# Performance work log

Measured on AMD Instinct MI355X. Metric: run time of the kernel, lower is better.

The kernel has to match this reference:

```python
import jax, jax.numpy as jnp
import numpy as np

TEMPERATURE = 0.5
EPS = 1e-8  # torch CosineSimilarity eps


def setup_inputs() -> dict:
    key = jax.random.key(0)
    k1, k2 = jax.random.split(key)
    N, D = 4096, 256
    z1 = jax.random.normal(k1, (N, D), dtype=jnp.float32)
    z2 = jax.random.normal(k2, (N, D), dtype=jnp.float32)
    return {"z1": z1, "z2": z2}


def reference(z1, z2):
    N = z1.shape[0]
    z = jnp.concatenate([z1, z2], axis=0)  # [2N, D]
    # cosine similarity = normalized dot products (GEMM instead of O(N^2 D) broadcast)
    norm = jnp.linalg.norm(z, axis=-1, keepdims=True)
    zn = z / jnp.maximum(norm, EPS)
    sim = (zn @ zn.T) / TEMPERATURE  # [2N, 2N]
    # mask self-similarity on the diagonal
    idx = jnp.arange(2 * N)
    sim = jnp.where(idx[:, None] == idx[None, :], -jnp.inf, sim)
    # target[i] = (i - N) mod 2N  (arange(2N).roll(N))
    target = jnp.roll(idx, N)
    logp = jax.nn.log_softmax(sim, axis=-1)
    loss = -jnp.mean(logp[idx, target])
    return loss
```

## Files before the change

### kernel.cpp

```cpp
#include <hip/hip_runtime.h>

typedef __bf16 bf16x8 __attribute__((ext_vector_type(8)));
typedef float f32x4 __attribute__((ext_vector_type(4)));

#define TWO_LOG2E 2.88539008177792681f

#define GLOADLDS16(g, l) __builtin_amdgcn_global_load_lds(                     \
    (const __attribute__((address_space(1))) void*)(g),                        \
    (__attribute__((address_space(3))) void*)(l), 16, 0, 0)

__device__ __forceinline__ unsigned short f2bf(float f) {
    unsigned int u = __float_as_uint(f);
    u = (u + 0x7FFFu + ((u >> 16) & 1u)) >> 16;
    return (unsigned short)u;
}

__global__ void normalize_kernel(const float* __restrict__ z1,
                                 const float* __restrict__ z2,
                                 unsigned short* __restrict__ zn) {
    const int wave = threadIdx.x >> 6, lane = threadIdx.x & 63;
    const int row = (blockIdx.x << 2) + wave;
    const float* src = (row < 4096) ? (z1 + row * 256) : (z2 + (row - 4096) * 256);
    float4 v = ((const float4*)src)[lane];
    float ss = v.x * v.x + v.y * v.y + v.z * v.z + v.w * v.w;
#pragma unroll
    for (int m = 32; m > 0; m >>= 1) ss += __shfl_xor(ss, m, 64);
    float scale = 1.0f / fmaxf(sqrtf(ss), 1e-8f);
    uint2 w;
    w.x = (unsigned)f2bf(v.x * scale) | ((unsigned)f2bf(v.y * scale) << 16);
    w.y = (unsigned)f2bf(v.z * scale) | ((unsigned)f2bf(v.w * scale) << 16);
    *(uint2*)(zn + row * 256 + (lane << 2)) = w;
}

__global__ void __launch_bounds__(256) simexp_kernel(
    const unsigned short* __restrict__ zn,
    float* __restrict__ S)
{
    __shared__ __align__(16) unsigned short As[128 * 64];
    __shared__ __align__(16) unsigned short Bs[128 * 64];

    const int tid  = threadIdx.x;
    const int lane = tid & 63;
    const int wave = tid >> 6;
    const int wr = wave >> 1;
    const int wc = wave & 1;
    const int q   = lane >> 4;
    const int n16 = lane & 15;

    int t = blockIdx.x, bi = 0;
    while (t >= 64 - bi) { t -= 64 - bi; ++bi; }
    const int bj = bi + t;
    const int rowBase = bi << 7;
    const int colBase = bj << 7;

    const int lrow = lane >> 3;
    const int k8s  = (lane & 7) ^ lrow;

    f32x4 acc[4][4];
#pragma unroll
    for (int i = 0; i < 4; ++i)
#pragma unroll
        for (int j = 0; j < 4; ++j) acc[i][j] = (f32x4){0.f, 0.f, 0.f, 0.f};

    for (int kc = 0; kc < 4; ++kc) {
        __syncthreads();
#pragma unroll
        for (int p = 0; p < 4; ++p) {
            const int seg = (wave << 2) + p;
            const int r = (seg << 3) + lrow;
            const unsigned short* ga = zn + ((rowBase + r) << 8) + (kc << 6) + (k8s << 3);
            const unsigned short* gb = zn + ((colBase + r) << 8) + (kc << 6) + (k8s << 3);
            GLOADLDS16(ga, As + (seg << 9) + (lane << 3));
            GLOADLDS16(gb, Bs + (seg << 9) + (lane << 3));
        }
        __syncthreads();
#pragma unroll
        for (int ks = 0; ks < 2; ++ks) {
            bf16x8 af[4], bfr[4];
#pragma unroll
            for (int rt = 0; rt < 4; ++rt) {
                const int ar = (wr << 6) + (rt << 4) + n16;
                const int kk = ((ks << 2) + q) ^ (n16 & 7);
                af[rt] = *(const bf16x8*)(As + (ar << 6) + (kk << 3));
            }
#pragma unroll
            for (int ct = 0; ct < 4; ++ct) {
                const int br = (wc << 6) + (ct << 4) + n16;
                const int kk = ((ks << 2) + q) ^ (n16 & 7);
                bfr[ct] = *(const bf16x8*)(Bs + (br << 6) + (kk << 3));
            }
#pragma unroll
            for (int rt = 0; rt < 4; ++rt)
#pragma unroll
                for (int ct = 0; ct < 4; ++ct)
                    acc[rt][ct] = __builtin_amdgcn_mfma_f32_16x16x32_bf16(
                        af[rt], bfr[ct], acc[rt][ct], 0, 0, 0);
        }
    }

    float rs[4][4];
    float cs[4];
#pragma unroll
    for (int i = 0; i < 4; ++i) {
        cs[i] = 0.f;
#pragma unroll
        for (int j = 0; j < 4; ++j) rs[i][j] = 0.f;
    }
#pragma unroll
    for (int rt = 0; rt < 4; ++rt)
#pragma unroll
        for (int ct = 0; ct < 4; ++ct)
#pragma unroll
            for (int r = 0; r < 4; ++r) {
                float e = __builtin_amdgcn_exp2f(acc[rt][ct][r] * TWO_LOG2E);
                rs[rt][r] += e;
                cs[ct] += e;
            }

#pragma unroll
    for (int rt = 0; rt < 4; ++rt)
#pragma unroll
        for (int r = 0; r < 4; ++r) {
            float s = rs[rt][r];
            s += __shfl_xor(s, 1, 64);
            s += __shfl_xor(s, 2, 64);
            s += __shfl_xor(s, 4, 64);
            s += __shfl_xor(s, 8, 64);
            if (n16 == 0) {
                int grow = rowBase + (wr << 6) + (rt << 4) + (q << 2) + r;
                atomicAdd(&S[grow], s);
            }
        }
    if (bi != bj) {
#pragma unroll
        for (int ct = 0; ct < 4; ++ct) {
            float s = cs[ct];
            s += __shfl_xor(s, 16, 64);
            s += __shfl_xor(s, 32, 64);
            if (q == 0) {
                int gcol = colBase + (wc << 6) + (ct << 4) + n16;
                atomicAdd(&S[gcol], s);
            }
        }
    }
}

__global__ void finish_kernel(const unsigned short* __restrict__ zn,
                              const float* __restrict__ S,
                              float* __restrict__ out)
{
    __shared__ float vals[16];
    const int tid = threadIdx.x, lane = tid & 63, wave = tid >> 6;
    const int rib = (wave << 2) + (lane >> 4);
    const int row = (blockIdx.x << 4) + rib;
    const int tar = (row + 4096) & 8191;
    const int l16 = lane & 15;

    float drr = 0.f, drt = 0.f;
#pragma unroll
    for (int i = 0; i < 4; ++i) {
        int k = (i << 6) + (l16 << 2);
        uint2 ur = *(const uint2*)(zn + (row << 8) + k);
        uint2 ut = *(const uint2*)(zn + (tar << 8) + k);
        float a0 = __uint_as_float(ur.x << 16);
        float a1 = __uint_as_float(ur.x & 0xFFFF0000u);
        float a2 = __uint_as_float(ur.y << 16);
        float a3 = __uint_as_float(ur.y & 0xFFFF0000u);
        float b0 = __uint_as_float(ut.x << 16);
        float b1 = __uint_as_float(ut.x & 0xFFFF0000u);
        float b2 = __uint_as_float(ut.y << 16);
        float b3 = __uint_as_float(ut.y & 0xFFFF0000u);
        drr += a0 * a0 + a1 * a1 + a2 * a2 + a3 * a3;
        drt += a0 * b0 + a1 * b1 + a2 * b2 + a3 * b3;
    }
#pragma unroll
    for (int m = 1; m <= 8; m <<= 1) {
        drr += __shfl_xor(drr, m, 64);
        drt += __shfl_xor(drt, m, 64);
    }
    if (l16 == 0) {
        float Sv = S[row] - __builtin_amdgcn_exp2f(drr * TWO_LOG2E);
        vals[rib] = 0.693147180559945f * __builtin_amdgcn_logf(Sv) - 2.0f * drt;
    }
    __syncthreads();
    if (tid == 0) {
        float s = 0.f;
#pragma unroll
        for (int i = 0; i < 16; ++i) s += vals[i];
        atomicAdd(out, s * (1.0f / 8192.0f));
    }
}

extern "C" void kernel_launch(void* const* d_in, const int* in_sizes, int n_in,
                              void* d_out, int out_size, void* d_ws, size_t ws_size,
                              hipStream_t stream)
{
    const float* z1 = (const float*)d_in[0];
    const float* z2 = (const float*)d_in[1];
    unsigned short* zn = (unsigned short*)d_ws;
    float* S = (float*)((char*)d_ws + 8192 * 256 * sizeof(unsigned short));
    float* out = (float*)d_out;

    hipMemsetAsync(S, 0, 8192 * sizeof(float), stream);
    hipMemsetAsync(out, 0, sizeof(float), stream);

    normalize_kernel<<<2048, 256, 0, stream>>>(z1, z2, zn);
    simexp_kernel<<<2080, 256, 0, stream>>>(zn, S);
    finish_kernel<<<512, 256, 0, stream>>>(zn, S, out);
}
```

Measured before the change: 126.0 us.

## Fuse normalize, similarity-exp, and finish into one persistent cooperative kernel

Replaces three kernel launches and two memsets with one cooperative persistent kernel that uses grid syncs between phases, with a non-cooperative fallback. The GEMM phase now gives each block a contiguous range of 128x64 upper-triangle tiles. A-rows stay in registers per strip, B tiles are double-buffered in LDS with prefetch, and row sums are flushed only on strip change, which cuts atomics. The aim is to remove launch and memset overhead and to improve load balance and latency hiding. In exchange it adds grid-sync costs, higher register pressure from holding A in registers, and host-side device queries on every call.

```diff
diff --git a/kernel.cpp b/kernel.cpp
--- a/kernel.cpp
+++ b/kernel.cpp
@@ -1,4 +1,7 @@
 #include <hip/hip_runtime.h>
+#include <hip/hip_cooperative_groups.h>
+
+namespace cg = cooperative_groups;
 
 typedef __bf16 bf16x8 __attribute__((ext_vector_type(8)));
 typedef float f32x4 __attribute__((ext_vector_type(4)));
@@ -9,186 +12,246 @@
     (const __attribute__((address_space(1))) void*)(g),                        \
     (__attribute__((address_space(3))) void*)(l), 16, 0, 0)
 
-__device__ __forceinline__ unsigned short f2bf(float f) {
-    unsigned int u = __float_as_uint(f);
-    u = (u + 0x7FFFu + ((u >> 16) & 1u)) >> 16;
-    return (unsigned short)u;
-}
-
-__global__ void normalize_kernel(const float* __restrict__ z1,
-                                 const float* __restrict__ z2,
-                                 unsigned short* __restrict__ zn) {
-    const int wave = threadIdx.x >> 6, lane = threadIdx.x & 63;
-    const int row = (blockIdx.x << 2) + wave;
-    const float* src = (row < 4096) ? (z1 + row * 256) : (z2 + (row - 4096) * 256);
-    float4 v = ((const float4*)src)[lane];
-    float ss = v.x * v.x + v.y * v.y + v.z * v.z + v.w * v.w;
-#pragma unroll
-    for (int m = 32; m > 0; m >>= 1) ss += __shfl_xor(ss, m, 64);
-    float scale = 1.0f / fmaxf(sqrtf(ss), 1e-8f);
-    uint2 w;
-    w.x = (unsigned)f2bf(v.x * scale) | ((unsigned)f2bf(v.y * scale) << 16);
-    w.y = (unsigned)f2bf(v.z * scale) | ((unsigned)f2bf(v.w * scale) << 16);
-    *(uint2*)(zn + row * 256 + (lane << 2)) = w;
-}
-
-__global__ void __launch_bounds__(256) simexp_kernel(
-    const unsigned short* __restrict__ zn,
-    float* __restrict__ S)
-{
-    __shared__ __align__(16) unsigned short As[128 * 64];
-    __shared__ __align__(16) unsigned short Bs[128 * 64];
-
-    const int tid  = threadIdx.x;
-    const int lane = tid & 63;
-    const int wave = tid >> 6;
-    const int wr = wave >> 1;
-    const int wc = wave & 1;
-    const int q   = lane >> 4;
-    const int n16 = lane & 15;
-
-    int t = blockIdx.x, bi = 0;
-    while (t >= 64 - bi) { t -= 64 - bi; ++bi; }
-    const int bj = bi + t;
-    const int rowBase = bi << 7;
-    const int colBase = bj << 7;
-
-    const int lrow = lane >> 3;
-    const int k8s  = (lane & 7) ^ lrow;
-
-    f32x4 acc[4][4];
+__device__ __forceinline__ unsigned f2bf(float f) {
+    unsigned u = __float_as_uint(f);
+    return (u + 0x7FFFu + ((u >> 16) & 1u)) >> 16;
+}
+
+__device__ __forceinline__ void phase1(const float* __restrict__ z1,
+                                       const float* __restrict__ z2,
+                                       unsigned short* __restrict__ zn,
+                                       float* __restrict__ S,
+                                       float* __restrict__ out) {
+    const int tid = threadIdx.x, lane = tid & 63, wave = tid >> 6;
+    for (int grp = blockIdx.x; grp < 512; grp += gridDim.x) {
+        if (tid < 16) S[(grp << 4) + tid] = 0.f;
+        if (grp == 0 && tid == 0) out[0] = 0.f;
+#pragma unroll
+        for (int r = 0; r < 4; ++r) {
+            int row = (grp << 4) + (wave << 2) + r;
+            const float* src = (row < 4096) ? (z1 + row * 256) : (z2 + (row - 4096) * 256);
+            float4 v = ((const float4*)src)[lane];
+            float ss = v.x * v.x + v.y * v.y + v.z * v.z + v.w * v.w;
+#pragma unroll
+            for (int m = 32; m > 0; m >>= 1) ss += __shfl_xor(ss, m, 64);
+            float sc = 1.0f / fmaxf(sqrtf(ss), 1e-8f);
+            uint2 w;
+            w.x = f2bf(v.x * sc) | (f2bf(v.y * sc) << 16);
+            w.y = f2bf(v.z * sc) | (f2bf(v.w * sc) << 16);
+            *(uint2*)(zn + row * 256 + (lane << 2)) = w;
+        }
+    }
+}
+
+__device__ __forceinline__ void phase2(const unsigned short* __restrict__ zn,
+                                       float* __restrict__ S,
+                                       unsigned short* __restrict__ Bs) {
+    const int tid = threadIdx.x, lane = tid & 63, wave = tid >> 6;
+    const int q = lane >> 4, n16 = lane & 15;
+    const int wr = wave >> 1, wc = wave & 1;
+    const int G = gridDim.x, b = blockIdx.x;
+
+    const int gs = (b * 4160) / G;
+    const int ge = ((b + 1) * 4160) / G;
+
+    int si = 0;
+    while ((si + 1) * (128 - si) <= gs) ++si;
+    int ti = gs - si * (129 - si);
+
+    auto stage = [&](int colBase, int h, int buf) {
+        unsigned short* base = Bs + (buf << 13);
+#pragma unroll
+        for (int p = 0; p < 4; ++p) {
+            int s16 = (p << 8) + tid;
+            int c   = s16 >> 4;
+            int k8  = (s16 & 15) ^ (c & 15);
+            GLOADLDS16(zn + ((colBase + c) << 8) + (h << 7) + (k8 << 3),
+                       base + (s16 << 3));
+        }
+    };
+
+    bf16x8 a[4][8];
+    auto loadA = [&](int rb) {
+#pragma unroll
+        for (int rt = 0; rt < 4; ++rt)
+#pragma unroll
+            for (int ks = 0; ks < 8; ++ks)
+                a[rt][ks] = *(const bf16x8*)(zn + ((rb + (wr << 6) + (rt << 4) + n16) << 8)
+                                                + (ks << 5) + (q << 3));
+    };
+
+    float rs[4][4];
 #pragma unroll
     for (int i = 0; i < 4; ++i)
 #pragma unroll
-        for (int j = 0; j < 4; ++j) acc[i][j] = (f32x4){0.f, 0.f, 0.f, 0.f};
-
-    for (int kc = 0; kc < 4; ++kc) {
-        __syncthreads();
-#pragma unroll
-        for (int p = 0; p < 4; ++p) {
-            const int seg = (wave << 2) + p;
-            const int r = (seg << 3) + lrow;
-            const unsigned short* ga = zn + ((rowBase + r) << 8) + (kc << 6) + (k8s << 3);
-            const unsigned short* gb = zn + ((colBase + r) << 8) + (kc << 6) + (k8s << 3);
-            GLOADLDS16(ga, As + (seg << 9) + (lane << 3));
-            GLOADLDS16(gb, Bs + (seg << 9) + (lane << 3));
-        }
-        __syncthreads();
-#pragma unroll
-        for (int ks = 0; ks < 2; ++ks) {
-            bf16x8 af[4], bfr[4];
-#pragma unroll
-            for (int rt = 0; rt < 4; ++rt) {
-                const int ar = (wr << 6) + (rt << 4) + n16;
-                const int kk = ((ks << 2) + q) ^ (n16 & 7);
-                af[rt] = *(const bf16x8*)(As + (ar << 6) + (kk << 3));
+        for (int j = 0; j < 4; ++j) rs[i][j] = 0.f;
+
+    auto flushRows = [&](int strip) {
+        int base = (strip << 7) + (wr << 6) + (q << 2);
+#pragma unroll
+        for (int rt = 0; rt < 4; ++rt)
+#pragma unroll
+            for (int r = 0; r < 4; ++r) {
+                float s = rs[rt][r];
+                s += __shfl_xor(s, 1, 64);
+                s += __shfl_xor(s, 2, 64);
+                s += __shfl_xor(s, 4, 64);
+                s += __shfl_xor(s, 8, 64);
+                if (n16 == 0) atomicAdd(&S[base + (rt << 4) + r], s);
+                rs[rt][r] = 0.f;
             }
-#pragma unroll
-            for (int ct = 0; ct < 4; ++ct) {
-                const int br = (wc << 6) + (ct << 4) + n16;
-                const int kk = ((ks << 2) + q) ^ (n16 & 7);
-                bfr[ct] = *(const bf16x8*)(Bs + (br << 6) + (kk << 3));
+    };
+
+    loadA(si << 7);
+    int curStrip = si;
+    stage((si << 7) + (ti << 6), 0, 0);
+    int pi = si, pt = ti, ph = 0;
+    int buf = 0;
+
+    for (int g = gs; g < ge; ++g) {
+        if (si != curStrip) { flushRows(curStrip); loadA(si << 7); curStrip = si; }
+        const int rowBase = si << 7;
+        const int colBase = rowBase + (ti << 6);
+
+        f32x4 acc[4][2];
+#pragma unroll
+        for (int rt = 0; rt < 4; ++rt)
+#pragma unroll
+            for (int ct = 0; ct < 2; ++ct) acc[rt][ct] = (f32x4){0.f, 0.f, 0.f, 0.f};
+
+#pragma unroll
+        for (int h = 0; h < 2; ++h) {
+            __syncthreads();
+            ph ^= 1;
+            if (ph == 0) { ++pt; if (pt >= 128 - (pi << 1)) { ++pi; pt = 0; } }
+            if (pi < 64) stage((pi << 7) + (pt << 6), ph, buf ^ 1);
+
+            const unsigned short* bb = Bs + (buf << 13);
+#pragma unroll
+            for (int ksl = 0; ksl < 4; ++ksl) {
+                bf16x8 bf[2];
+#pragma unroll
+                for (int ct = 0; ct < 2; ++ct) {
+                    int c  = (wc << 5) + (ct << 4) + n16;
+                    int k8 = ((ksl << 2) | q) ^ n16;
+                    bf[ct] = *(const bf16x8*)(bb + (((c << 4) | k8) << 3));
+                }
+#pragma unroll
+                for (int rt = 0; rt < 4; ++rt)
+#pragma unroll
+                    for (int ct = 0; ct < 2; ++ct)
+                        acc[rt][ct] = __builtin_amdgcn_mfma_f32_16x16x32_bf16(
+                            a[rt][(h << 2) + ksl], bf[ct], acc[rt][ct], 0, 0, 0);
             }
-#pragma unroll
-            for (int rt = 0; rt < 4; ++rt)
-#pragma unroll
-                for (int ct = 0; ct < 4; ++ct)
-                    acc[rt][ct] = __builtin_amdgcn_mfma_f32_16x16x32_bf16(
-                        af[rt], bfr[ct], acc[rt][ct], 0, 0, 0);
-        }
-    }
-
-    float rs[4][4];
-    float cs[4];
-#pragma unroll
-    for (int i = 0; i < 4; ++i) {
-        cs[i] = 0.f;
-#pragma unroll
-        for (int j = 0; j < 4; ++j) rs[i][j] = 0.f;
-    }
-#pragma unroll
-    for (int rt = 0; rt < 4; ++rt)
-#pragma unroll
-        for (int ct = 0; ct < 4; ++ct)
-#pragma unroll
-            for (int r = 0; r < 4; ++r) {
-                float e = __builtin_amdgcn_exp2f(acc[rt][ct][r] * TWO_LOG2E);
-                rs[rt][r] += e;
-                cs[ct] += e;
-            }
-
-#pragma unroll
-    for (int rt = 0; rt < 4; ++rt)
-#pragma unroll
-        for (int r = 0; r < 4; ++r) {
-            float s = rs[rt][r];
-            s += __shfl_xor(s, 1, 64);
-            s += __shfl_xor(s, 2, 64);
-            s += __shfl_xor(s, 4, 64);
-            s += __shfl_xor(s, 8, 64);
-            if (n16 == 0) {
-                int grow = rowBase + (wr << 6) + (rt << 4) + (q << 2) + r;
-                atomicAdd(&S[grow], s);
-            }
-        }
-    if (bi != bj) {
-#pragma unroll
-        for (int ct = 0; ct < 4; ++ct) {
+            buf ^= 1;
+        }
+
+        float cs[2] = {0.f, 0.f};
+        const bool strad = (ti < 2);
+        const int ibase = rowBase + (wr << 6) + (q << 2);
+        const int jb    = colBase + (wc << 5) + n16;
+#pragma unroll
+        for (int rt = 0; rt < 4; ++rt)
+#pragma unroll
+            for (int ct = 0; ct < 2; ++ct)
+#pragma unroll
+                for (int r = 0; r < 4; ++r) {
+                    float e = __builtin_amdgcn_exp2f(acc[rt][ct][r] * TWO_LOG2E);
+                    if (strad) {
+                        int ii = ibase + (rt << 4) + r;
+                        int jj = jb + (ct << 4);
+                        rs[rt][r] += (jj >= ii) ? e : 0.f;
+                        cs[ct]    += (jj >  ii) ? e : 0.f;
+                    } else {
+                        rs[rt][r] += e;
+                        cs[ct]    += e;
+                    }
+                }
+#pragma unroll
+        for (int ct = 0; ct < 2; ++ct) {
             float s = cs[ct];
             s += __shfl_xor(s, 16, 64);
             s += __shfl_xor(s, 32, 64);
-            if (q == 0) {
-                int gcol = colBase + (wc << 6) + (ct << 4) + n16;
-                atomicAdd(&S[gcol], s);
-            }
-        }
-    }
-}
-
-__global__ void finish_kernel(const unsigned short* __restrict__ zn,
-                              const float* __restrict__ S,
-                              float* __restrict__ out)
+            if (q == 0) atomicAdd(&S[colBase + (wc << 5) + (ct << 4) + n16], s);
+        }
+        ++ti; if (ti >= 128 - (si << 1)) { ++si; ti = 0; }
+    }
+    flushRows(curStrip);
+}
+
+__device__ __forceinline__ void phase3(const unsigned short* __restrict__ zn,
+                                       const float* __restrict__ S,
+                                       float* __restrict__ out,
+                                       float* __restrict__ vals) {
+    const int tid = threadIdx.x, lane = tid & 63, wave = tid >> 6;
+    const int q = lane >> 4, n16 = lane & 15;
+    const int rib = (wave << 2) + q;
+    for (int grp = blockIdx.x; grp < 512; grp += gridDim.x) {
+        int row = (grp << 4) + rib;
+        int tar = (row + 4096) & 8191;
+        float drr = 0.f, drt = 0.f;
+#pragma unroll
+        for (int i = 0; i < 4; ++i) {
+            int k = (i << 6) + (n16 << 2);
+            uint2 ur = *(const uint2*)(zn + (row << 8) + k);
+            uint2 ut = *(const uint2*)(zn + (tar << 8) + k);
+            float a0 = __uint_as_float(ur.x << 16),  a1 = __uint_as_float(ur.x & 0xFFFF0000u);
+            float a2 = __uint_as_float(ur.y << 16),  a3 = __uint_as_float(ur.y & 0xFFFF0000u);
+            float b0 = __uint_as_float(ut.x << 16),  b1 = __uint_as_float(ut.x & 0xFFFF0000u);
+            float b2 = __uint_as_float(ut.y << 16),  b3 = __uint_as_float(ut.y & 0xFFFF0000u);
+            drr += a0 * a0 + a1 * a1 + a2 * a2 + a3 * a3;
+            drt += a0 * b0 + a1 * b1 + a2 * b2 + a3 * b3;
+        }
+#pragma unroll
+        for (int m = 1; m <= 8; m <<= 1) {
+            drr += __shfl_xor(drr, m, 64);
+            drt += __shfl_xor(drt, m, 64);
+        }
+        __syncthreads();
+        if (n16 == 0) {
+            float Sv = S[row] - __builtin_amdgcn_exp2f(drr * TWO_LOG2E);
+            vals[rib] = 0.693147180559945f * __builtin_amdgcn_logf(Sv) - 2.0f * drt;
+        }
+        __syncthreads();
+        if (tid == 0) {
+            float s = 0.f;
+#pragma unroll
+            for (int i = 0; i < 16; ++i) s += vals[i];
+            atomicAdd(out, s * (1.0f / 8192.0f));
+        }
+    }
+}
+
+__global__ void __launch_bounds__(256, 2) ntxent_fused(
+    const float* __restrict__ z1, const float* __restrict__ z2,
+    unsigned short* __restrict__ zn, float* __restrict__ S, float* __restrict__ out)
+{
+    __shared__ __align__(16) unsigned short Bs[2][8192];
+    phase1(z1, z2, zn, S, out);
+    cg::this_grid().sync();
+    phase2(zn, S, &Bs[0][0]);
+    cg::this_grid().sync();
+    phase3(zn, S, out, (float*)&Bs[0][0]);
+}
+
+__global__ void __launch_bounds__(256, 2) norm_k(
+    const float* __restrict__ z1, const float* __restrict__ z2,
+    unsigned short* __restrict__ zn, float* __restrict__ S, float* __restrict__ out)
+{ phase1(z1, z2, zn, S, out); }
+
+__global__ void __launch_bounds__(256, 2) simexp_k(
+    const unsigned short* __restrict__ zn, float* __restrict__ S)
+{
+    __shared__ __align__(16) unsigned short Bs[2][8192];
+    phase2(zn, S, &Bs[0][0]);
+}
+
+__global__ void __launch_bounds__(256, 2) finish_k(
+    const unsigned short* __restrict__ zn, const float* __restrict__ S,
+    float* __restrict__ out)
 {
     __shared__ float vals[16];
-    const int tid = threadIdx.x, lane = tid & 63, wave = tid >> 6;
-    const int rib = (wave << 2) + (lane >> 4);
-    const int row = (blockIdx.x << 4) + rib;
-    const int tar = (row + 4096) & 8191;
-    const int l16 = lane & 15;
-
-    float drr = 0.f, drt = 0.f;
-#pragma unroll
-    for (int i = 0; i < 4; ++i) {
-        int k = (i << 6) + (l16 << 2);
-        uint2 ur = *(const uint2*)(zn + (row << 8) + k);
-        uint2 ut = *(const uint2*)(zn + (tar << 8) + k);
-        float a0 = __uint_as_float(ur.x << 16);
-        float a1 = __uint_as_float(ur.x & 0xFFFF0000u);
-        float a2 = __uint_as_float(ur.y << 16);
-        float a3 = __uint_as_float(ur.y & 0xFFFF0000u);
-        float b0 = __uint_as_float(ut.x << 16);
-        float b1 = __uint_as_float(ut.x & 0xFFFF0000u);
-        float b2 = __uint_as_float(ut.y << 16);
-        float b3 = __uint_as_float(ut.y & 0xFFFF0000u);
-        drr += a0 * a0 + a1 * a1 + a2 * a2 + a3 * a3;
-        drt += a0 * b0 + a1 * b1 + a2 * b2 + a3 * b3;
-    }
-#pragma unroll
-    for (int m = 1; m <= 8; m <<= 1) {
-        drr += __shfl_xor(drr, m, 64);
-        drt += __shfl_xor(drt, m, 64);
-    }
-    if (l16 == 0) {
-        float Sv = S[row] - __builtin_amdgcn_exp2f(drr * TWO_LOG2E);
-        vals[rib] = 0.693147180559945f * __builtin_amdgcn_logf(Sv) - 2.0f * drt;
-    }
-    __syncthreads();
-    if (tid == 0) {
-        float s = 0.f;
-#pragma unroll
-        for (int i = 0; i < 16; ++i) s += vals[i];
-        atomicAdd(out, s * (1.0f / 8192.0f));
-    }
+    phase3(zn, S, out, vals);
 }
 
 extern "C" void kernel_launch(void* const* d_in, const int* in_sizes, int n_in,
@@ -201,10 +264,25 @@
     float* S = (float*)((char*)d_ws + 8192 * 256 * sizeof(unsigned short));
     float* out = (float*)d_out;
 
-    hipMemsetAsync(S, 0, 8192 * sizeof(float), stream);
-    hipMemsetAsync(out, 0, sizeof(float), stream);
-
-    normalize_kernel<<<2048, 256, 0, stream>>>(z1, z2, zn);
-    simexp_kernel<<<2080, 256, 0, stream>>>(zn, S);
-    finish_kernel<<<512, 256, 0, stream>>>(zn, S, out);
-}
+    int dev = 0;
+    hipGetDevice(&dev);
+    int coopOK = 0;
+    hipDeviceGetAttribute(&coopOK, hipDeviceAttributeCooperativeLaunch, dev);
+    int cus = 0;
+    hipDeviceGetAttribute(&cus, hipDeviceAttributeMultiprocessorCount, dev);
+    int maxB = 0;
+    hipOccupancyMaxActiveBlocksPerMultiprocessor(&maxB, ntxent_fused, 256, 0);
+
+    long long cap = (long long)maxB * (long long)cus;
+    int G = (cap >= 512) ? 512 : (int)cap;
+
+    if (coopOK && G >= 256) {
+        void* args[] = {(void*)&z1, (void*)&z2, (void*)&zn, (void*)&S, (void*)&out};
+        hipError_t err = hipLaunchCooperativeKernel(ntxent_fused, dim3(G), dim3(256),
+                                                    args, 0, stream);
+        if (err == hipSuccess) return;
+    }
+    norm_k<<<512, 256, 0, stream>>>(z1, z2, zn, S, out);
+    simexp_k<<<512, 256, 0, stream>>>(zn, S);
+    finish_k<<<512, 256, 0, stream>>>(zn, S, out);
+}
```

Measured after the change: 261.0 us. 2.07x slower.
